# Optimization experiments

Hardware: AMD Instinct MI355X
Metric: run time of the kernel (lower is better)

Reference implementation:

```python
import jax, jax.numpy as jnp
import numpy as np

H = 100          # hidden size (hard-coded in module)
B, C, T = 256, 9, 1024
NC = 6           # num_classes


def _lstm_layer(xs, W_ih, W_hh, b, h0, c0):
    """xs: [B,T,In] -> hidden sequence [B,T,H]. Torch gate order i,f,g,o."""
    # Precompute the input projection for all timesteps in one big GEMM.
    pre = jnp.einsum('bti,gi->btg', xs, W_ih) + b   # [B,T,4H]
    pre_t = jnp.swapaxes(pre, 0, 1)                 # [T,B,4H]

    def step(carry, p):
        h, c = carry
        g = p + h @ W_hh.T                          # [B,4H]
        i, f, gg, o = jnp.split(g, 4, axis=-1)
        c = jax.nn.sigmoid(f) * c + jax.nn.sigmoid(i) * jnp.tanh(gg)
        h = jax.nn.sigmoid(o) * jnp.tanh(c)
        return (h, c), h

    (_, _), hs = jax.lax.scan(step, (h0, c0), pre_t)
    return jnp.swapaxes(hs, 0, 1)                   # [B,T,H]


def setup_inputs() -> dict:
    key = jax.random.key(0)
    ks = jax.random.split(key, 14)
    s = 0.1  # ~ uniform(-1/sqrt(H), 1/sqrt(H)) scale of torch default init
    n = lambda k, shape, sc=s: jax.random.normal(k, shape, dtype=jnp.float32) * sc
    return {
        'x':     jax.random.normal(ks[0], (B, C, T), dtype=jnp.float32),
        'h0_1':  jax.random.normal(ks[1], (B, H), dtype=jnp.float32),
        'c0_1':  jax.random.normal(ks[2], (B, H), dtype=jnp.float32),
        'h0_2':  jax.random.normal(ks[3], (B, H), dtype=jnp.float32),
        'c0_2':  jax.random.normal(ks[4], (B, H), dtype=jnp.float32),
        'W_ih1': n(ks[5], (4 * H, C)),
        'W_hh1': n(ks[6], (4 * H, H)),
        'b1':    n(ks[7], (4 * H,)),   # b_ih + b_hh folded together
        'W_ih2': n(ks[8], (4 * H, H)),
        'W_hh2': n(ks[9], (4 * H, H)),
        'b2':    n(ks[10], (4 * H,)),
        'W_fc':  n(ks[11], (NC, H)),
        'b_fc':  n(ks[12], (NC,)),
    }


def reference(x, h0_1, c0_1, h0_2, c0_2, W_ih1, W_hh1, b1,
              W_ih2, W_hh2, b2, W_fc, b_fc):
    xs = jnp.swapaxes(x, 1, 2)                      # [B,T,C] (x.transpose(1,2))
    h1 = _lstm_layer(xs, W_ih1, W_hh1, b1, h0_1, c0_1)   # [B,T,H]
    h2 = _lstm_layer(h1, W_ih2, W_hh2, b2, h0_2, c0_2)   # [B,T,H]
    out = h2[:, -1, :] @ W_fc.T + b_fc              # [B,NC]
    return out
```

## Files before the change

### kernel.cpp

```cpp
#include <hip/hip_runtime.h>

#define HH   100
#define G4   400
#define BB   256
#define CC   9
#define TT   1024
#define NCLS 6
#define XSTR 13

__device__ __forceinline__ float sigm(float x) {
    return __fdividef(1.0f, 1.0f + __expf(-x));
}
__device__ __forceinline__ float tanh_fast(float x) {
    return 2.0f * sigm(2.0f * x) - 1.0f;
}
__device__ __forceinline__ float bcast(float v, int l) {
    return __int_as_float(__builtin_amdgcn_readlane(__float_as_int(v), l));
}

__global__ __launch_bounds__(448, 1)
void lstm_layer1(const float* __restrict__ x,
                 const float* __restrict__ h0,
                 const float* __restrict__ c0,
                 const float* __restrict__ W_ih,
                 const float* __restrict__ W_hh,
                 const float* __restrict__ bias_g,
                 float* __restrict__ h1out)
{
    const int b    = blockIdx.x;
    const int tid  = threadIdx.x;
    const int lane = tid & 63;

    __shared__ float xT[TT * XSTR + 64];
    __shared__ float hb[128];
    __shared__ float gates[448];

    const float* xb = x + (size_t)b * CC * TT;
    for (int i = tid; i < CC * TT; i += 448) {
        int c  = i >> 10;
        int tp = i & 1023;
        xT[tp * XSTR + c] = xb[i];
    }
    if (tid < 128) hb[tid] = (tid < HH) ? h0[b * HH + tid] : 0.0f;
    float c_reg = (tid < HH) ? c0[b * HH + tid] : 0.0f;

    const int row = (tid < G4) ? tid : 0;
    float w_ih[CC], w_hh[HH], bg;
    #pragma unroll
    for (int j = 0; j < CC; ++j) w_ih[j] = W_ih[row * CC + j];
    #pragma unroll
    for (int j = 0; j < HH; ++j) w_hh[j] = W_hh[row * HH + j];
    bg = bias_g[row];
    const bool isG = (row >= 2 * HH && row < 3 * HH);
    float* hout = h1out + (size_t)b * TT * HH;
    __syncthreads();

    for (int t = 0; t < TT; ++t) {
        float vx = xT[t * XSTR + lane];
        float va = hb[lane];
        float vb = hb[64 + lane];
        asm volatile("" : "+v"(vx), "+v"(va), "+v"(vb));

        float a0 = bg, a1 = 0.f, a2 = 0.f, a3 = 0.f;
        #pragma unroll
        for (int c = 0; c < CC; ++c) {
            float h_ = bcast(vx, c);
            if ((c & 3) == 0) a0 += h_ * w_ih[c];
            else if ((c & 3) == 1) a1 += h_ * w_ih[c];
            else if ((c & 3) == 2) a2 += h_ * w_ih[c];
            else a3 += h_ * w_ih[c];
        }
        #pragma unroll
        for (int j = 0; j < 64; ++j) {
            float h_ = bcast(va, j);
            if ((j & 3) == 0) a0 += h_ * w_hh[j];
            else if ((j & 3) == 1) a1 += h_ * w_hh[j];
            else if ((j & 3) == 2) a2 += h_ * w_hh[j];
            else a3 += h_ * w_hh[j];
        }
        #pragma unroll
        for (int j = 0; j < 36; ++j) {
            float h_ = bcast(vb, j);
            if ((j & 3) == 0) a0 += h_ * w_hh[64 + j];
            else if ((j & 3) == 1) a1 += h_ * w_hh[64 + j];
            else if ((j & 3) == 2) a2 += h_ * w_hh[64 + j];
            else a3 += h_ * w_hh[64 + j];
        }
        float raw = (a0 + a1) + (a2 + a3);
        float xv  = isG ? 2.0f * raw : raw;
        float s   = sigm(xv);
        gates[tid] = isG ? (2.0f * s - 1.0f) : s;

        __syncthreads();
        if (tid < HH) {
            float gi = gates[tid];
            float gf = gates[tid + HH];
            float gg = gates[tid + 2 * HH];
            float go = gates[tid + 3 * HH];
            float cc = gf * c_reg + gi * gg;
            c_reg = cc;
            float hv = go * tanh_fast(cc);
            hb[tid] = hv;
            hout[t * HH + tid] = hv;
        }
        __syncthreads();
    }
}

__global__ __launch_bounds__(512, 1)
void lstm_layer2_fc(const float* __restrict__ h1,
                    const float* __restrict__ h0,
                    const float* __restrict__ c0,
                    const float* __restrict__ W_ih,
                    const float* __restrict__ W_hh,
                    const float* __restrict__ bias_g,
                    const float* __restrict__ W_fc,
                    const float* __restrict__ b_fc,
                    float* __restrict__ out)
{
    const int b    = blockIdx.x;
    const int tid  = threadIdx.x;
    const int lane = tid & 63;

    __shared__ float h1buf[2][128];
    __shared__ float h2b[128];
    __shared__ float gates[448];

    if (tid < 128) {
        h2b[tid] = (tid < HH) ? h0[b * HH + tid] : 0.0f;
        h1buf[0][tid] = 0.0f;
        h1buf[1][tid] = 0.0f;
    }
    float c_reg = (tid < HH) ? c0[b * HH + tid] : 0.0f;

    const int row = (tid < G4) ? tid : 0;
    float w_ih[HH], w_hh[HH], bg;
    #pragma unroll
    for (int j = 0; j < HH; ++j) w_ih[j] = W_ih[row * HH + j];
    #pragma unroll
    for (int j = 0; j < HH; ++j) w_hh[j] = W_hh[row * HH + j];
    bg = bias_g[row];
    const bool isG = (row >= 2 * HH && row < 3 * HH);
    const float* h1b = h1 + (size_t)b * TT * HH;
    __syncthreads();

    if (tid >= 448 && tid < 448 + HH / 4) {
        int i = tid - 448;
        ((float4*)h1buf[0])[i] = ((const float4*)h1b)[i];
    }
    __syncthreads();

    for (int t = 0; t < TT; ++t) {
        const int cur = t & 1;
        if (tid < 448) {
            float va = h1buf[cur][lane];
            float vb = h1buf[cur][64 + lane];
            float vc = h2b[lane];
            float vd = h2b[64 + lane];
            asm volatile("" : "+v"(va), "+v"(vb), "+v"(vc), "+v"(vd));

            float a0 = bg, a1 = 0.f, a2 = 0.f, a3 = 0.f;
            #pragma unroll
            for (int j = 0; j < 64; ++j) {
                float h_ = bcast(va, j);
                if ((j & 3) == 0) a0 += h_ * w_ih[j];
                else if ((j & 3) == 1) a1 += h_ * w_ih[j];
                else if ((j & 3) == 2) a2 += h_ * w_ih[j];
                else a3 += h_ * w_ih[j];
            }
            #pragma unroll
            for (int j = 0; j < 36; ++j) {
                float h_ = bcast(vb, j);
                if ((j & 3) == 0) a0 += h_ * w_ih[64 + j];
                else if ((j & 3) == 1) a1 += h_ * w_ih[64 + j];
                else if ((j & 3) == 2) a2 += h_ * w_ih[64 + j];
                else a3 += h_ * w_ih[64 + j];
            }
            #pragma unroll
            for (int j = 0; j < 64; ++j) {
                float h_ = bcast(vc, j);
                if ((j & 3) == 0) a0 += h_ * w_hh[j];
                else if ((j & 3) == 1) a1 += h_ * w_hh[j];
                else if ((j & 3) == 2) a2 += h_ * w_hh[j];
                else a3 += h_ * w_hh[j];
            }
            #pragma unroll
            for (int j = 0; j < 36; ++j) {
                float h_ = bcast(vd, j);
                if ((j & 3) == 0) a0 += h_ * w_hh[64 + j];
                else if ((j & 3) == 1) a1 += h_ * w_hh[64 + j];
                else if ((j & 3) == 2) a2 += h_ * w_hh[64 + j];
                else a3 += h_ * w_hh[64 + j];
            }
            float raw = (a0 + a1) + (a2 + a3);
            float xv  = isG ? 2.0f * raw : raw;
            float s   = sigm(xv);
            gates[tid] = isG ? (2.0f * s - 1.0f) : s;
        } else if ((t + 1) < TT && tid < 448 + HH / 4) {
            int i = tid - 448;
            ((float4*)h1buf[cur ^ 1])[i] = ((const float4*)(h1b + (t + 1) * HH))[i];
        }
        __syncthreads();
        if (tid < HH) {
            float gi = gates[tid];
            float gf = gates[tid + HH];
            float gg = gates[tid + 2 * HH];
            float go = gates[tid + 3 * HH];
            float cc = gf * c_reg + gi * gg;
            c_reg = cc;
            h2b[tid] = go * tanh_fast(cc);
        }
        __syncthreads();
    }

    if (tid < NCLS) {
        float acc = b_fc[tid];
        #pragma unroll 4
        for (int j = 0; j < HH; ++j) acc += W_fc[tid * HH + j] * h2b[j];
        out[b * NCLS + tid] = acc;
    }
}

extern "C" void kernel_launch(void* const* d_in, const int* in_sizes, int n_in,
                              void* d_out, int out_size, void* d_ws, size_t ws_size,
                              hipStream_t stream) {
    const float* x     = (const float*)d_in[0];
    const float* h0_1  = (const float*)d_in[1];
    const float* c0_1  = (const float*)d_in[2];
    const float* h0_2  = (const float*)d_in[3];
    const float* c0_2  = (const float*)d_in[4];
    const float* W_ih1 = (const float*)d_in[5];
    const float* W_hh1 = (const float*)d_in[6];
    const float* b1    = (const float*)d_in[7];
    const float* W_ih2 = (const float*)d_in[8];
    const float* W_hh2 = (const float*)d_in[9];
    const float* b2    = (const float*)d_in[10];
    const float* W_fc  = (const float*)d_in[11];
    const float* b_fc  = (const float*)d_in[12];
    float* out = (float*)d_out;

    float* h1 = (float*)d_ws;

    lstm_layer1<<<BB, 448, 0, stream>>>(x, h0_1, c0_1, W_ih1, W_hh1, b1, h1);
    lstm_layer2_fc<<<BB, 512, 0, stream>>>(h1, h0_2, c0_2, W_ih2, W_hh2, b2,
                                           W_fc, b_fc, out);
}
```

Baseline: 2.345 ms.

## Split each gate row's dot product across two thread halves to shorten recurrence

Each LSTM block now has twice as many threads. Each gate row's dot product is split between two threads: the input-projection part plus half of the recurrent part, and the remaining recurrent part (layer 2 splits W_ih and W_hh). The two partial sums go to shared memory and are added by the cell-update threads, which now also apply the sigmoid and tanh activations. The goal is to halve the serial readlane/FMA chain per timestep and the registers each thread holds. In exchange it adds extra shared-memory traffic, duplicated activation work in the update threads, and larger blocks that take more wavefronts to synchronise at each barrier.

```diff
diff --git a/kernel.cpp b/kernel.cpp
--- a/kernel.cpp
+++ b/kernel.cpp
@@ -18,7 +18,7 @@
     return __int_as_float(__builtin_amdgcn_readlane(__float_as_int(v), l));
 }
 
-__global__ __launch_bounds__(448, 1)
+__global__ __launch_bounds__(896, 2)
 void lstm_layer1(const float* __restrict__ x,
                  const float* __restrict__ h0,
                  const float* __restrict__ c0,
@@ -33,10 +33,10 @@
 
     __shared__ float xT[TT * XSTR + 64];
     __shared__ float hb[128];
-    __shared__ float gates[448];
+    __shared__ float p[2][448];
 
     const float* xb = x + (size_t)b * CC * TT;
-    for (int i = tid; i < CC * TT; i += 448) {
+    for (int i = tid; i < CC * TT; i += 896) {
         int c  = i >> 10;
         int tp = i & 1023;
         xT[tp * XSTR + c] = xb[i];
@@ -44,62 +44,65 @@
     if (tid < 128) hb[tid] = (tid < HH) ? h0[b * HH + tid] : 0.0f;
     float c_reg = (tid < HH) ? c0[b * HH + tid] : 0.0f;
 
-    const int row = (tid < G4) ? tid : 0;
-    float w_ih[CC], w_hh[HH], bg;
+    const bool half0 = (tid < 448);
+    const int  r     = half0 ? tid : (tid - 448);
+    const int  row   = (r < G4) ? r : 0;
+
+    float w[55], bg = 0.0f;
+    if (half0) {
+        #pragma unroll
+        for (int j = 0; j < CC; ++j) w[j] = W_ih[row * CC + j];
+        #pragma unroll
+        for (int j = 0; j < 46; ++j) w[CC + j] = W_hh[row * HH + j];
+        bg = bias_g[row];
+    } else {
+        #pragma unroll
+        for (int j = 0; j < 54; ++j) w[j] = W_hh[row * HH + 46 + j];
+        w[54] = 0.0f;
+    }
     #pragma unroll
-    for (int j = 0; j < CC; ++j) w_ih[j] = W_ih[row * CC + j];
-    #pragma unroll
-    for (int j = 0; j < HH; ++j) w_hh[j] = W_hh[row * HH + j];
-    bg = bias_g[row];
-    const bool isG = (row >= 2 * HH && row < 3 * HH);
+    for (int j = 0; j < 55; ++j) asm volatile("" : "+v"(w[j]));
+
     float* hout = h1out + (size_t)b * TT * HH;
     __syncthreads();
 
     for (int t = 0; t < TT; ++t) {
-        float vx = xT[t * XSTR + lane];
-        float va = hb[lane];
-        float vb = hb[64 + lane];
-        asm volatile("" : "+v"(vx), "+v"(va), "+v"(vb));
-
-        float a0 = bg, a1 = 0.f, a2 = 0.f, a3 = 0.f;
-        #pragma unroll
-        for (int c = 0; c < CC; ++c) {
-            float h_ = bcast(vx, c);
-            if ((c & 3) == 0) a0 += h_ * w_ih[c];
-            else if ((c & 3) == 1) a1 += h_ * w_ih[c];
-            else if ((c & 3) == 2) a2 += h_ * w_ih[c];
-            else a3 += h_ * w_ih[c];
-        }
-        #pragma unroll
-        for (int j = 0; j < 64; ++j) {
-            float h_ = bcast(va, j);
-            if ((j & 3) == 0) a0 += h_ * w_hh[j];
-            else if ((j & 3) == 1) a1 += h_ * w_hh[j];
-            else if ((j & 3) == 2) a2 += h_ * w_hh[j];
-            else a3 += h_ * w_hh[j];
-        }
-        #pragma unroll
-        for (int j = 0; j < 36; ++j) {
-            float h_ = bcast(vb, j);
-            if ((j & 3) == 0) a0 += h_ * w_hh[64 + j];
-            else if ((j & 3) == 1) a1 += h_ * w_hh[64 + j];
-            else if ((j & 3) == 2) a2 += h_ * w_hh[64 + j];
-            else a3 += h_ * w_hh[64 + j];
-        }
-        float raw = (a0 + a1) + (a2 + a3);
-        float xv  = isG ? 2.0f * raw : raw;
-        float s   = sigm(xv);
-        gates[tid] = isG ? (2.0f * s - 1.0f) : s;
-
+        if (half0) {
+            float vx = xT[t * XSTR + lane];
+            float va = hb[lane];
+            asm volatile("" : "+v"(vx), "+v"(va));
+            float a0 = bg, a1 = 0.f;
+            #pragma unroll
+            for (int c = 0; c < CC; ++c) {
+                float h_ = bcast(vx, c);
+                if (c & 1) a1 += h_ * w[c]; else a0 += h_ * w[c];
+            }
+            #pragma unroll
+            for (int j = 0; j < 46; ++j) {
+                float h_ = bcast(va, j);
+                if (j & 1) a1 += h_ * w[CC + j]; else a0 += h_ * w[CC + j];
+            }
+            p[0][tid] = a0 + a1;
+        } else {
+            float vb = hb[46 + lane];
+            asm volatile("" : "+v"(vb));
+            float a0 = 0.f, a1 = 0.f;
+            #pragma unroll
+            for (int j = 0; j < 54; ++j) {
+                float h_ = bcast(vb, j);
+                if (j & 1) a1 += h_ * w[j]; else a0 += h_ * w[j];
+            }
+            p[1][tid - 448] = a0 + a1;
+        }
         __syncthreads();
         if (tid < HH) {
-            float gi = gates[tid];
-            float gf = gates[tid + HH];
-            float gg = gates[tid + 2 * HH];
-            float go = gates[tid + 3 * HH];
-            float cc = gf * c_reg + gi * gg;
+            float ri = p[0][tid]          + p[1][tid];
+            float rf = p[0][tid + HH]     + p[1][tid + HH];
+            float rg = p[0][tid + 2 * HH] + p[1][tid + 2 * HH];
+            float ro = p[0][tid + 3 * HH] + p[1][tid + 3 * HH];
+            float cc = sigm(rf) * c_reg + sigm(ri) * tanh_fast(rg);
             c_reg = cc;
-            float hv = go * tanh_fast(cc);
+            float hv = sigm(ro) * tanh_fast(cc);
             hb[tid] = hv;
             hout[t * HH + tid] = hv;
         }
@@ -107,7 +110,7 @@
     }
 }
 
-__global__ __launch_bounds__(512, 1)
+__global__ __launch_bounds__(960, 2)
 void lstm_layer2_fc(const float* __restrict__ h1,
                     const float* __restrict__ h0,
                     const float* __restrict__ c0,
@@ -124,7 +127,7 @@
 
     __shared__ float h1buf[2][128];
     __shared__ float h2b[128];
-    __shared__ float gates[448];
+    __shared__ float p[2][448];
 
     if (tid < 128) {
         h2b[tid] = (tid < HH) ? h0[b * HH + tid] : 0.0f;
@@ -133,82 +136,65 @@
     }
     float c_reg = (tid < HH) ? c0[b * HH + tid] : 0.0f;
 
-    const int row = (tid < G4) ? tid : 0;
-    float w_ih[HH], w_hh[HH], bg;
+    const bool comp  = (tid < 896);
+    const bool half0 = (tid < 448);
+    const int  r     = half0 ? tid : (tid - 448);
+    const int  row   = (r < G4) ? r : 0;
+
+    float w[HH], bg = 0.0f;
+    {
+        const float* wsrc = half0 ? (W_ih + row * HH) : (W_hh + row * HH);
+        #pragma unroll
+        for (int j = 0; j < HH; ++j) w[j] = wsrc[j];
+        if (half0) bg = bias_g[row];
+    }
     #pragma unroll
-    for (int j = 0; j < HH; ++j) w_ih[j] = W_ih[row * HH + j];
-    #pragma unroll
-    for (int j = 0; j < HH; ++j) w_hh[j] = W_hh[row * HH + j];
-    bg = bias_g[row];
-    const bool isG = (row >= 2 * HH && row < 3 * HH);
+    for (int j = 0; j < HH; ++j) asm volatile("" : "+v"(w[j]));
+
     const float* h1b = h1 + (size_t)b * TT * HH;
     __syncthreads();
 
-    if (tid >= 448 && tid < 448 + HH / 4) {
-        int i = tid - 448;
-        ((float4*)h1buf[0])[i] = ((const float4*)h1b)[i];
+    if (tid >= 896) {
+        int i = tid - 896;
+        if (i < HH / 4)
+            ((float4*)h1buf[0])[i] = ((const float4*)h1b)[i];
     }
     __syncthreads();
 
     for (int t = 0; t < TT; ++t) {
         const int cur = t & 1;
-        if (tid < 448) {
-            float va = h1buf[cur][lane];
-            float vb = h1buf[cur][64 + lane];
-            float vc = h2b[lane];
-            float vd = h2b[64 + lane];
-            asm volatile("" : "+v"(va), "+v"(vb), "+v"(vc), "+v"(vd));
-
-            float a0 = bg, a1 = 0.f, a2 = 0.f, a3 = 0.f;
+        if (comp) {
+            const float* hsrc = half0 ? h1buf[cur] : h2b;
+            float va = hsrc[lane];
+            float vb = hsrc[64 + lane];
+            asm volatile("" : "+v"(va), "+v"(vb));
+            float a0 = bg, a1 = 0.f;
             #pragma unroll
             for (int j = 0; j < 64; ++j) {
                 float h_ = bcast(va, j);
-                if ((j & 3) == 0) a0 += h_ * w_ih[j];
-                else if ((j & 3) == 1) a1 += h_ * w_ih[j];
-                else if ((j & 3) == 2) a2 += h_ * w_ih[j];
-                else a3 += h_ * w_ih[j];
+                if (j & 1) a1 += h_ * w[j]; else a0 += h_ * w[j];
             }
             #pragma unroll
             for (int j = 0; j < 36; ++j) {
                 float h_ = bcast(vb, j);
-                if ((j & 3) == 0) a0 += h_ * w_ih[64 + j];
-                else if ((j & 3) == 1) a1 += h_ * w_ih[64 + j];
-                else if ((j & 3) == 2) a2 += h_ * w_ih[64 + j];
-                else a3 += h_ * w_ih[64 + j];
-            }
-            #pragma unroll
-            for (int j = 0; j < 64; ++j) {
-                float h_ = bcast(vc, j);
-                if ((j & 3) == 0) a0 += h_ * w_hh[j];
-                else if ((j & 3) == 1) a1 += h_ * w_hh[j];
-                else if ((j & 3) == 2) a2 += h_ * w_hh[j];
-                else a3 += h_ * w_hh[j];
-            }
-            #pragma unroll
-            for (int j = 0; j < 36; ++j) {
-                float h_ = bcast(vd, j);
-                if ((j & 3) == 0) a0 += h_ * w_hh[64 + j];
-                else if ((j & 3) == 1) a1 += h_ * w_hh[64 + j];
-                else if ((j & 3) == 2) a2 += h_ * w_hh[64 + j];
-                else a3 += h_ * w_hh[64 + j];
-            }
-            float raw = (a0 + a1) + (a2 + a3);
-            float xv  = isG ? 2.0f * raw : raw;
-            float s   = sigm(xv);
-            gates[tid] = isG ? (2.0f * s - 1.0f) : s;
-        } else if ((t + 1) < TT && tid < 448 + HH / 4) {
-            int i = tid - 448;
-            ((float4*)h1buf[cur ^ 1])[i] = ((const float4*)(h1b + (t + 1) * HH))[i];
+                if (j & 1) a1 += h_ * w[64 + j]; else a0 += h_ * w[64 + j];
+            }
+            p[half0 ? 0 : 1][r] = a0 + a1;
+        } else if ((t + 1) < TT) {
+            int i = tid - 896;
+            if (i < HH / 4)
+                ((float4*)h1buf[cur ^ 1])[i] =
+                    ((const float4*)(h1b + (t + 1) * HH))[i];
         }
         __syncthreads();
         if (tid < HH) {
-            float gi = gates[tid];
-            float gf = gates[tid + HH];
-            float gg = gates[tid + 2 * HH];
-            float go = gates[tid + 3 * HH];
-            float cc = gf * c_reg + gi * gg;
+            float ri = p[0][tid]          + p[1][tid];
+            float rf = p[0][tid + HH]     + p[1][tid + HH];
+            float rg = p[0][tid + 2 * HH] + p[1][tid + 2 * HH];
+            float ro = p[0][tid + 3 * HH] + p[1][tid + 3 * HH];
+            float cc = sigm(rf) * c_reg + sigm(ri) * tanh_fast(rg);
             c_reg = cc;
-            h2b[tid] = go * tanh_fast(cc);
+            h2b[tid] = sigm(ro) * tanh_fast(cc);
         }
         __syncthreads();
     }
@@ -241,7 +227,7 @@
 
     float* h1 = (float*)d_ws;
 
-    lstm_layer1<<<BB, 448, 0, stream>>>(x, h0_1, c0_1, W_ih1, W_hh1, b1, h1);
-    lstm_layer2_fc<<<BB, 512, 0, stream>>>(h1, h0_2, c0_2, W_ih2, W_hh2, b2,
+    lstm_layer1<<<BB, 896, 0, stream>>>(x, h0_1, c0_1, W_ih1, W_hh1, b1, h1);
+    lstm_layer2_fc<<<BB, 960, 0, stream>>>(h1, h0_2, c0_2, W_ih2, W_hh2, b2,
                                            W_fc, b_fc, out);
 }
```

Result: slower. 2.500 ms (+6.6%).
